# Optimization experiments

Hardware: AMD Instinct MI355X
Metric: run time of the kernel (lower is better)

The kernel has to match this reference:

```python
import jax, jax.numpy as jnp
import numpy as np

N = 50000   # nodes
E = 800000  # edges (avg degree 16)
IN = 128
HID = 128
OUT = 64    # num classes


def setup_inputs() -> dict:
    key = jax.random.key(0)
    ks = jax.random.split(key, 10)
    x = jax.random.normal(ks[0], (N, IN), dtype=jnp.float32)
    edge_src = jax.random.randint(ks[1], (E,), 0, N)
    edge_dst = jax.random.randint(ks[2], (E,), 0, N)
    y = jax.random.randint(ks[3], (N,), 0, OUT)
    train_mask = jax.random.bernoulli(ks[4], 0.5, (N,))
    w = lambda k, sh: (jax.random.normal(k, sh, dtype=jnp.float32) * (1.0 / np.sqrt(sh[0]))).astype(jnp.float32)
    return dict(
        x=x, edge_src=edge_src, edge_dst=edge_dst, y=y, train_mask=train_mask,
        W1l=w(ks[5], (IN, HID)), b1=jnp.zeros((HID,), jnp.float32), W1r=w(ks[6], (IN, HID)),
        W2l=w(ks[7], (HID, OUT)), b2=jnp.zeros((OUT,), jnp.float32), W2r=w(ks[8], (HID, OUT)),
    )


def mean_aggr(h, src, dst, n):
    # sparse adjacency matmul with reduce='mean': for each dst node, mean of src features
    msg_sum = jax.ops.segment_sum(h[src], dst, num_segments=n)          # [N, D]
    cnt = jax.ops.segment_sum(jnp.ones((src.shape[0],), h.dtype), dst, num_segments=n)
    return msg_sum / jnp.maximum(cnt, 1.0)[:, None]


def reference(x, edge_src, edge_dst, y, train_mask, W1l, b1, W1r, W2l, b2, W2r):
    n = x.shape[0]
    # dropout(p=0.2, training=False) is identity in eval mode
    h = x
    # layer 1: SAGEConv = lin_l(mean_aggr(h)) + lin_r(h), then ReLU (+identity dropout)
    a = mean_aggr(h, edge_src, edge_dst, n)
    h = jax.nn.relu(a @ W1l + b1 + h @ W1r)
    # layer 2 (output layer)
    a = mean_aggr(h, edge_src, edge_dst, n)
    logits = a @ W2l + b2 + h @ W2r
    logp = jax.nn.log_softmax(logits, axis=1)
    # nll_loss over masked nodes (single chunk => loss / num_chunks with num_chunks=1)
    m = train_mask.astype(logp.dtype)
    nll = -jnp.take_along_axis(logp, y[:, None], axis=1)[:, 0]
    loss = jnp.sum(nll * m) / jnp.maximum(jnp.sum(m), 1.0)
    return loss
```

## Files before the change

### kernel.cpp

```cpp
#include <hip/hip_runtime.h>
#include <hip/hip_bf16.h>

typedef unsigned int uint;
typedef unsigned short u16;

#define DIN 128
#define DHID 128
#define DOUT 64
#define BSH 8
#define P3CHUNK 8192
#define P4MAX 6144

static inline size_t al256(size_t x) { return (x + 255) & ~(size_t)255; }

typedef __attribute__((ext_vector_type(8))) short short8;
typedef __attribute__((ext_vector_type(4))) float floatx4;
typedef __attribute__((ext_vector_type(2))) float floatx2;
typedef __attribute__((ext_vector_type(4))) int intx4;

__device__ inline float2 bf2x(uint v) {
    return make_float2(__uint_as_float(v << 16), __uint_as_float(v & 0xffff0000u));
}
__device__ inline uint packbf(float a, float b) {
    uint ua = __float_as_uint(a), ub = __float_as_uint(b);
    ua += 0x7fff + ((ua >> 16) & 1);
    ub += 0x7fff + ((ub >> 16) & 1);
    return (ua >> 16) | (ub & 0xffff0000u);
}
__device__ inline u16 pb(float a) {
    uint u = __float_as_uint(a);
    u += 0x7fff + ((u >> 16) & 1);
    return (u16)(u >> 16);
}

__device__ inline floatx2 f8lo(uint v) {
#if __has_builtin(__builtin_amdgcn_cvt_pk_f32_fp8)
    return __builtin_amdgcn_cvt_pk_f32_fp8((int)v, false);
#else
    uint b0 = v & 0xffu, b1 = (v >> 8) & 0xffu;
    floatx2 r;
    r.x = __uint_as_float(((b0 & 0x80u) << 24) | ((b0 & 0x7fu) << 20)) * 0x1p120f;
    r.y = __uint_as_float(((b1 & 0x80u) << 24) | ((b1 & 0x7fu) << 20)) * 0x1p120f;
    return r;
#endif
}
__device__ inline floatx2 f8hi(uint v) {
#if __has_builtin(__builtin_amdgcn_cvt_pk_f32_fp8)
    return __builtin_amdgcn_cvt_pk_f32_fp8((int)v, true);
#else
    uint b0 = (v >> 16) & 0xffu, b1 = (v >> 24) & 0xffu;
    floatx2 r;
    r.x = __uint_as_float(((b0 & 0x80u) << 24) | ((b0 & 0x7fu) << 20)) * 0x1p120f;
    r.y = __uint_as_float(((b1 & 0x80u) << 24) | ((b1 & 0x7fu) << 20)) * 0x1p120f;
    return r;
#endif
}
__device__ inline uint enc8(float f) {
    uint ub = __float_as_uint(f * 0x1p-120f);
    uint s = (ub >> 24) & 0x80u;
    uint mag = ub & 0x7fffffffu;
    mag += 0x7ffffu + ((mag >> 20) & 1u);
    uint r = mag >> 20;
    if (r > 0x7eu) r = 0x7eu;
    return r | s;
}
__device__ inline uint packf8x4(float a, float b, float c, float d) {
#if __has_builtin(__builtin_amdgcn_cvt_pk_fp8_f32)
    int p = __builtin_amdgcn_cvt_pk_fp8_f32(a, b, 0, false);
    p = __builtin_amdgcn_cvt_pk_fp8_f32(c, d, p, true);
    return (uint)p;
#else
    return enc8(a) | (enc8(b) << 8) | (enc8(c) << 16) | (enc8(d) << 24);
#endif
}

__global__ __launch_bounds__(256) void pack_detect_bhist_kernel(
    const float* __restrict__ W1l, const float* __restrict__ W1r,
    const float* __restrict__ W2l, const float* __restrict__ W2r,
    u16* __restrict__ Wp1, u16* __restrict__ Wp2,
    const int* __restrict__ tm, int n_int, int* __restrict__ gflags,
    const int* __restrict__ dst, int e, int nb, uint* __restrict__ bcounts) {
    __shared__ uint lh[512];
    int bx = blockIdx.x;
    if (bx < 192) {
        int id = bx * 256 + threadIdx.x;
        if (id < 32768) {
            int frag = id >> 9, el = id & 511;
            int lane = el >> 3, j = el & 7;
            int kc = frag >> 4, tn = frag & 15;
            int k = kc * 32 + (lane >> 4) * 8 + j;
            int ncol = tn * 16 + (lane & 15);
            float v = (ncol < 128) ? W1l[k * 128 + ncol] : W1r[k * 128 + ncol - 128];
            Wp1[id] = pb(v);
        } else if (id < 49152) {
            int id2 = id - 32768;
            int frag = id2 >> 9, el = id2 & 511;
            int lane = el >> 3, j = el & 7;
            int kc = frag >> 3, tn = frag & 7;
            int k = kc * 32 + (lane >> 4) * 8 + j;
            int ncol = tn * 16 + (lane & 15);
            float v = (ncol < 64) ? W2l[k * 64 + ncol] : W2r[k * 64 + ncol - 64];
            Wp2[id2] = pb(v);
        }
    } else if (bx < 256) {
        int i = (bx - 192) * 256 + threadIdx.x;
        bool hf = false, ho = false;
        for (; i < n_int; i += 64 * 256) {
            int v = tm[i];
            hf |= (v == 0x3F800000);
            ho |= (v != 0 && v != 1 && v != 0x3F800000);
        }
        if (__any(hf) && (threadIdx.x & 63) == 0) atomicOr(&gflags[0], 1);
        if (__any(ho) && (threadIdx.x & 63) == 0) atomicOr(&gflags[1], 1);
    } else {
        for (int i = threadIdx.x; i < 512; i += 256) lh[i] = 0;
        __syncthreads();
        int nquad = (e + 3) >> 2;
        for (int i = (bx - 256) * 256 + threadIdx.x; i < nquad; i += 256 * 256) {
            int base = i * 4;
            if (base + 4 <= e) {
                intx4 d = __builtin_nontemporal_load((const intx4*)(dst + base));
                atomicAdd(&lh[d.x >> BSH], 1u);
                atomicAdd(&lh[d.y >> BSH], 1u);
                atomicAdd(&lh[d.z >> BSH], 1u);
                atomicAdd(&lh[d.w >> BSH], 1u);
            } else {
                for (int k = base; k < e; ++k) atomicAdd(&lh[dst[k] >> BSH], 1u);
            }
        }
        __syncthreads();
        for (int i = threadIdx.x; i < nb; i += 256) {
            uint c = lh[i];
            if (c) atomicAdd(&bcounts[i], c);
        }
    }
}

__global__ __launch_bounds__(256) void bscan_kernel(const uint* __restrict__ bcounts, int nb, int e,
                                                    uint* __restrict__ bbase, uint* __restrict__ bcursor,
                                                    int* __restrict__ offsets, int n) {
    __shared__ uint pws[4];
    int t = threadIdx.x;
    uint v0 = (2 * t < nb) ? bcounts[2 * t] : 0u;
    uint v1 = (2 * t + 1 < nb) ? bcounts[2 * t + 1] : 0u;
    uint s = v0 + v1;
    int lane = t & 63, wv = t >> 6;
    uint incl = s;
    #pragma unroll
    for (int d = 1; d < 64; d <<= 1) {
        uint u = (uint)__shfl_up((int)incl, d, 64);
        if (lane >= d) incl += u;
    }
    if (lane == 63) pws[wv] = incl;
    __syncthreads();
    uint woff = 0;
    #pragma unroll
    for (int i = 0; i < 4; ++i) if (i < wv) woff += pws[i];
    uint excl = woff + incl - s;
    if (2 * t < nb) { bbase[2 * t] = excl; bcursor[2 * t] = excl; }
    if (2 * t + 1 < nb) { bbase[2 * t + 1] = excl + v0; bcursor[2 * t + 1] = excl + v0; }
    if (t == 0) {
        uint tot = pws[0] + pws[1] + pws[2] + pws[3];
        bbase[nb] = tot;
        offsets[n] = e;
    }
}

__global__ __launch_bounds__(256) void partition_kernel(const int* __restrict__ src,
                                                        const int* __restrict__ dst, int e, int nb,
                                                        uint* __restrict__ bcursor,
                                                        uint* __restrict__ pairs) {
    __shared__ uint lh[512], lexcl[512], lbase[512], lpos[512];
    __shared__ uint st[P3CHUNK];
    __shared__ uint pws[4];
    int t = threadIdx.x;
    int e0 = blockIdx.x * P3CHUNK;
    int ecnt = min(P3CHUNK, e - e0);
    for (int i = t; i < 512; i += 256) { lh[i] = 0; lpos[i] = 0; }
    __syncthreads();
    for (int i = t; i < ecnt; i += 256)
        atomicAdd(&lh[dst[e0 + i] >> BSH], 1u);
    __syncthreads();
    {
        uint v0 = lh[2 * t], v1 = lh[2 * t + 1];
        uint s = v0 + v1;
        int lane = t & 63, wv = t >> 6;
        uint incl = s;
        #pragma unroll
        for (int d = 1; d < 64; d <<= 1) {
            uint u = (uint)__shfl_up((int)incl, d, 64);
            if (lane >= d) incl += u;
        }
        if (lane == 63) pws[wv] = incl;
        __syncthreads();
        uint woff = 0;
        #pragma unroll
        for (int i = 0; i < 4; ++i) if (i < wv) woff += pws[i];
        uint excl = woff + incl - s;
        lexcl[2 * t] = excl;
        lexcl[2 * t + 1] = excl + v0;
    }
    __syncthreads();
    for (int b = t; b < nb; b += 256) {
        uint c = lh[b];
        lbase[b] = c ? atomicAdd(&bcursor[b], c) : 0u;
    }
    __syncthreads();
    for (int i = t; i < ecnt; i += 256) {
        int d = dst[e0 + i];
        int s = src[e0 + i];
        int b = d >> BSH;
        uint slot = lexcl[b] + atomicAdd(&lpos[b], 1u);
        st[slot] = ((uint)(d & ((1 << BSH) - 1)) << 16) | (uint)s;
    }
    __syncthreads();
    int wv = t >> 6, lane = t & 63;
    for (int b = wv; b < nb; b += 4) {
        uint c = lh[b];
        uint lsrc = lexcl[b], gdst = lbase[b];
        for (uint k = lane; k < c; k += 64)
            pairs[gdst + k] = st[lsrc + k];
    }
}

__global__ __launch_bounds__(256) void emit_gemm1_kernel(
    const uint* __restrict__ pairs, const uint* __restrict__ bbase,
    u16* __restrict__ csr, int* __restrict__ offsets, int nb_emit,
    const float* __restrict__ X, const u16* __restrict__ Wp1,
    const float* __restrict__ b1,
    uint* __restrict__ P1f8, uint* __restrict__ Q1u, int n) {
    __shared__ u16 smem[4][16][260];
    int t = threadIdx.x;
    if (blockIdx.x < nb_emit) {
        uint* cnt = (uint*)&smem[0][0][0];
        uint* lex = cnt + 256;
        uint* pws = lex + 256;
        u16* ob = (u16*)(pws + 8);
        int b = blockIdx.x;
        uint seg0 = bbase[b];
        int len = (int)(bbase[b + 1] - seg0);
        int n0 = b << BSH;
        cnt[t] = 0;
        __syncthreads();
        for (int i = t; i < len; i += 256)
            atomicAdd(&cnt[pairs[seg0 + i] >> 16], 1u);
        __syncthreads();
        uint v = cnt[t];
        int lane = t & 63, wv = t >> 6;
        uint incl = v;
        #pragma unroll
        for (int d = 1; d < 64; d <<= 1) {
            uint u = (uint)__shfl_up((int)incl, d, 64);
            if (lane >= d) incl += u;
        }
        if (lane == 63) pws[wv] = incl;
        __syncthreads();
        uint woff = 0;
        #pragma unroll
        for (int i = 0; i < 4; ++i) if (i < wv) woff += pws[i];
        uint excl = woff + incl - v;
        lex[t] = excl;
        if (n0 + t < n) offsets[n0 + t] = (int)(seg0 + excl);
        __syncthreads();
        cnt[t] = 0;
        __syncthreads();
        for (int i = t; i < len; i += 256) {
            uint p = pairs[seg0 + i];
            uint loc = p >> 16;
            uint slot = lex[loc] + atomicAdd(&cnt[loc], 1u);
            if (slot < P4MAX) ob[slot] = (u16)(p & 0xffffu);
            else csr[seg0 + slot] = (u16)(p & 0xffffu);
        }
        __syncthreads();
        int lim = min(len, P4MAX);
        for (int i = t; i < lim; i += 256) csr[seg0 + i] = ob[i];
        return;
    }
    int bid = blockIdx.x - nb_emit;
    int w = t >> 6, lane = t & 63;
    int q = lane >> 4, c = lane & 15;
    int m0 = bid * 128 + w * 32;
    int meA = min(m0 + c, n - 1);
    int meB = min(m0 + 16 + c, n - 1);
    const float* xrowA = X + (size_t)meA * 128 + q * 8;
    const float* xrowB = X + (size_t)meB * 128 + q * 8;
    const u16* wbase = Wp1 + lane * 8;

    floatx4 acc[2][16];
    #pragma unroll
    for (int h = 0; h < 2; ++h)
        #pragma unroll
        for (int i = 0; i < 16; ++i) acc[h][i] = (floatx4){0.f, 0.f, 0.f, 0.f};

    #pragma unroll
    for (int kc = 0; kc < 4; ++kc) {
        float4 xa0 = *(const float4*)(xrowA + kc * 32);
        float4 xa1 = *(const float4*)(xrowA + kc * 32 + 4);
        float4 xb0 = *(const float4*)(xrowB + kc * 32);
        float4 xb1 = *(const float4*)(xrowB + kc * 32 + 4);
        union { short8 s; uint4 u; } a0, a1;
        a0.u.x = packbf(xa0.x, xa0.y); a0.u.y = packbf(xa0.z, xa0.w);
        a0.u.z = packbf(xa1.x, xa1.y); a0.u.w = packbf(xa1.z, xa1.w);
        a1.u.x = packbf(xb0.x, xb0.y); a1.u.y = packbf(xb0.z, xb0.w);
        a1.u.z = packbf(xb1.x, xb1.y); a1.u.w = packbf(xb1.z, xb1.w);
        #pragma unroll
        for (int tn = 0; tn < 16; ++tn) {
            union { short8 s; uint4 u; } b;
            b.u = *(const uint4*)(wbase + (kc * 16 + tn) * 512);
            acc[0][tn] = __builtin_amdgcn_mfma_f32_16x16x32_bf16(a0.s, b.s, acc[0][tn], 0, 0, 0);
            acc[1][tn] = __builtin_amdgcn_mfma_f32_16x16x32_bf16(a1.s, b.s, acc[1][tn], 0, 0, 0);
        }
    }

    #pragma unroll
    for (int h = 0; h < 2; ++h) {
        #pragma unroll
        for (int tn = 0; tn < 16; ++tn) {
            int col = tn * 16 + c;
            float badd = (tn >= 8) ? b1[col - 128] : 0.f;
            #pragma unroll
            for (int i = 0; i < 4; ++i)
                smem[w][q * 4 + i][col] = pb(acc[h][tn][i] + badd);
        }
        int r0 = m0 + h * 16;
        for (int r = 0; r < 16; ++r) {
            int grow = r0 + r;
            if (grow >= n) continue;
            uint2 v = *(const uint2*)&smem[w][r][lane * 4];
            if (lane < 32) {
                float2 e0 = bf2x(v.x), e1 = bf2x(v.y);
                P1f8[(size_t)grow * 32 + lane] = packf8x4(e0.x, e0.y, e1.x, e1.y);
            } else {
                *(uint2*)&Q1u[(size_t)grow * 64 + 2 * (lane - 32)] = v;
            }
        }
    }
}

__global__ __launch_bounds__(256) void hist_kernel(const int* __restrict__ dst, int e,
                                                   int* __restrict__ counts) {
    int base = (blockIdx.x * 256 + threadIdx.x) * 4;
    if (base + 4 <= e) {
        intx4 d = __builtin_nontemporal_load((const intx4*)(dst + base));
        atomicAdd(&counts[d.x], 1);
        atomicAdd(&counts[d.y], 1);
        atomicAdd(&counts[d.z], 1);
        atomicAdd(&counts[d.w], 1);
    } else {
        for (int i = base; i < e; ++i) atomicAdd(&counts[dst[i]], 1);
    }
}

__global__ __launch_bounds__(256) void scan_partial_kernel(const int* __restrict__ counts, int n,
                                                           int* __restrict__ partials) {
    int t = threadIdx.x;
    int base = blockIdx.x * 1024 + t * 4;
    int s = 0;
    if (base + 3 < n) {
        int4 v = *(const int4*)&counts[base];
        s = v.x + v.y + v.z + v.w;
    } else {
        for (int i = 0; i < 4; ++i) if (base + i < n) s += counts[base + i];
    }
    #pragma unroll
    for (int d = 32; d; d >>= 1) s += __shfl_down(s, d, 64);
    __shared__ int wsum[4];
    if ((t & 63) == 0) wsum[t >> 6] = s;
    __syncthreads();
    if (t == 0) partials[blockIdx.x] = wsum[0] + wsum[1] + wsum[2] + wsum[3];
}

__global__ void scan_top_kernel(int* __restrict__ partials, int nparts, int* __restrict__ total_out) {
    int lane = threadIdx.x;
    int v = (lane < nparts) ? partials[lane] : 0;
    int incl = v;
    #pragma unroll
    for (int d = 1; d < 64; d <<= 1) {
        int u = __shfl_up(incl, d, 64);
        if (lane >= d) incl += u;
    }
    if (lane < nparts) partials[lane] = incl - v;
    if (lane == 63) *total_out = incl;
}

__global__ __launch_bounds__(256) void scan_final_kernel(const int* __restrict__ counts, int n,
                                                         const int* __restrict__ partials,
                                                         int* __restrict__ offsets,
                                                         int* __restrict__ cursor) {
    int t = threadIdx.x;
    int base = blockIdx.x * 1024 + t * 4;
    int v0 = 0, v1 = 0, v2 = 0, v3 = 0;
    if (base + 3 < n) {
        int4 q = *(const int4*)&counts[base];
        v0 = q.x; v1 = q.y; v2 = q.z; v3 = q.w;
    } else {
        if (base + 0 < n) v0 = counts[base + 0];
        if (base + 1 < n) v1 = counts[base + 1];
        if (base + 2 < n) v2 = counts[base + 2];
        if (base + 3 < n) v3 = counts[base + 3];
    }
    int s = v0 + v1 + v2 + v3;
    int lane = t & 63, wid = t >> 6;
    int incl = s;
    #pragma unroll
    for (int d = 1; d < 64; d <<= 1) {
        int u = __shfl_up(incl, d, 64);
        if (lane >= d) incl += u;
    }
    __shared__ int wsum[4];
    if (lane == 63) wsum[wid] = incl;
    __syncthreads();
    int woff = 0;
    #pragma unroll
    for (int i = 0; i < 4; ++i) if (i < wid) woff += wsum[i];
    int run = partials[blockIdx.x] + woff + incl - s;
    if (base + 0 < n) { offsets[base + 0] = run; cursor[base + 0] = run; run += v0; }
    if (base + 1 < n) { offsets[base + 1] = run; cursor[base + 1] = run; run += v1; }
    if (base + 2 < n) { offsets[base + 2] = run; cursor[base + 2] = run; run += v2; }
    if (base + 3 < n) { offsets[base + 3] = run; cursor[base + 3] = run; run += v3; }
}

__global__ __launch_bounds__(256) void scatter_kernel(const int* __restrict__ src,
                                                      const int* __restrict__ dst, int e,
                                                      int* __restrict__ cursor,
                                                      uint* __restrict__ csr_src) {
    int base = (blockIdx.x * 256 + threadIdx.x) * 4;
    if (base + 4 <= e) {
        intx4 s = __builtin_nontemporal_load((const intx4*)(src + base));
        intx4 d = __builtin_nontemporal_load((const intx4*)(dst + base));
        int p0 = atomicAdd(&cursor[d.x], 1);
        int p1 = atomicAdd(&cursor[d.y], 1);
        int p2 = atomicAdd(&cursor[d.z], 1);
        int p3 = atomicAdd(&cursor[d.w], 1);
        csr_src[p0] = (uint)s.x;
        csr_src[p1] = (uint)s.y;
        csr_src[p2] = (uint)s.z;
        csr_src[p3] = (uint)s.w;
    } else {
        for (int i = base; i < e; ++i) {
            int p = atomicAdd(&cursor[dst[i]], 1);
            csr_src[p] = (uint)src[i];
        }
    }
}

template <typename IT>
__global__ __launch_bounds__(256) void aggr1_kernel(
    const uint* __restrict__ P1f8, const uint* __restrict__ Q1u,
    const int* __restrict__ offsets, const IT* __restrict__ csr,
    uint* __restrict__ h1u, int n) {
    int node = (int)((blockIdx.x * (size_t)blockDim.x + threadIdx.x) >> 6);
    int lane = threadIdx.x & 63;
    int l = lane & 31, hw = lane >> 5;
    if (node >= n) return;
    int beg = offsets[node], end = offsets[node + 1];
    float a0 = 0.f, a1 = 0.f, a2 = 0.f, a3 = 0.f;
    int i = beg + hw;
    for (; i + 6 < end; i += 8) {
        int s0 = csr[i], s1 = csr[i + 2], s2 = csr[i + 4], s3 = csr[i + 6];
        uint v0 = P1f8[(size_t)s0 * 32 + l];
        uint v1 = P1f8[(size_t)s1 * 32 + l];
        uint v2 = P1f8[(size_t)s2 * 32 + l];
        uint v3 = P1f8[(size_t)s3 * 32 + l];
        floatx2 u0 = f8lo(v0), w0 = f8hi(v0);
        floatx2 u1 = f8lo(v1), w1 = f8hi(v1);
        floatx2 u2 = f8lo(v2), w2 = f8hi(v2);
        floatx2 u3 = f8lo(v3), w3 = f8hi(v3);
        a0 += (u0.x + u1.x) + (u2.x + u3.x);
        a1 += (u0.y + u1.y) + (u2.y + u3.y);
        a2 += (w0.x + w1.x) + (w2.x + w3.x);
        a3 += (w0.y + w1.y) + (w2.y + w3.y);
    }
    for (; i < end; i += 2) {
        int s = csr[i];
        uint v = P1f8[(size_t)s * 32 + l];
        floatx2 u = f8lo(v), w2 = f8hi(v);
        a0 += u.x; a1 += u.y; a2 += w2.x; a3 += w2.y;
    }
    a0 += __shfl_xor(a0, 32, 64);
    a1 += __shfl_xor(a1, 32, 64);
    a2 += __shfl_xor(a2, 32, 64);
    a3 += __shfl_xor(a3, 32, 64);
    if (hw == 0) {
        float inv = 1.0f / (float)max(end - beg, 1);
        uint2 qv = *(const uint2*)&Q1u[(size_t)node * 64 + l * 2];
        float2 q0 = bf2x(qv.x), q1 = bf2x(qv.y);
        float r0 = fmaxf(fmaf(a0, inv, q0.x), 0.f);
        float r1 = fmaxf(fmaf(a1, inv, q0.y), 0.f);
        float r2 = fmaxf(fmaf(a2, inv, q1.x), 0.f);
        float r3 = fmaxf(fmaf(a3, inv, q1.y), 0.f);
        uint2 o;
        o.x = packbf(r0, r1);
        o.y = packbf(r2, r3);
        *(uint2*)&h1u[(size_t)node * 64 + l * 2] = o;
    }
}

__global__ __launch_bounds__(256) void gemm2_mfma(
    const uint* __restrict__ H1u, const u16* __restrict__ Wp2,
    const float* __restrict__ b2,
    uint* __restrict__ P2f8, uint* __restrict__ Q2u, int n) {
    __shared__ u16 ep[4][16][132];
    int t = threadIdx.x;
    int w = t >> 6, lane = t & 63;
    int q = lane >> 4, c = lane & 15;
    int m0 = blockIdx.x * 128 + w * 32;
    int meA = min(m0 + c, n - 1);
    int meB = min(m0 + 16 + c, n - 1);
    const u16* hrowA = (const u16*)H1u + (size_t)meA * 128 + q * 8;
    const u16* hrowB = (const u16*)H1u + (size_t)meB * 128 + q * 8;
    const u16* wbase = Wp2 + lane * 8;

    floatx4 acc[2][8];
    #pragma unroll
    for (int h = 0; h < 2; ++h)
        #pragma unroll
        for (int i = 0; i < 8; ++i) acc[h][i] = (floatx4){0.f, 0.f, 0.f, 0.f};

    #pragma unroll
    for (int kc = 0; kc < 4; ++kc) {
        union { short8 s; uint4 u; } a0, a1;
        a0.u = *(const uint4*)(hrowA + kc * 32);
        a1.u = *(const uint4*)(hrowB + kc * 32);
        #pragma unroll
        for (int tn = 0; tn < 8; ++tn) {
            union { short8 s; uint4 u; } b;
            b.u = *(const uint4*)(wbase + (kc * 8 + tn) * 512);
            acc[0][tn] = __builtin_amdgcn_mfma_f32_16x16x32_bf16(a0.s, b.s, acc[0][tn], 0, 0, 0);
            acc[1][tn] = __builtin_amdgcn_mfma_f32_16x16x32_bf16(a1.s, b.s, acc[1][tn], 0, 0, 0);
        }
    }

    #pragma unroll
    for (int h = 0; h < 2; ++h) {
        #pragma unroll
        for (int tn = 0; tn < 8; ++tn) {
            int col = tn * 16 + c;
            float badd = (tn >= 4) ? b2[col - 64] : 0.f;
            #pragma unroll
            for (int i = 0; i < 4; ++i)
                ep[w][q * 4 + i][col] = pb(acc[h][tn][i] + badd);
        }
        int r0 = m0 + h * 16;
        for (int r = 0; r < 16; ++r) {
            int grow = r0 + r;
            if (grow >= n) continue;
            if (lane < 16) {
                uint2 v = *(const uint2*)&ep[w][r][lane * 4];
                float2 e0 = bf2x(v.x), e1 = bf2x(v.y);
                P2f8[(size_t)grow * 16 + lane] = packf8x4(e0.x, e0.y, e1.x, e1.y);
            } else if (lane < 48) {
                uint v = *(const uint*)&ep[w][r][64 + (lane - 16) * 2];
                Q2u[(size_t)grow * 32 + (lane - 16)] = v;
            }
        }
    }
}

template <typename IT>
__global__ __launch_bounds__(1024) void loss_kernel(
    const uint* __restrict__ P2f8, const uint* __restrict__ Q2u,
    const int* __restrict__ offsets, const IT* __restrict__ csr,
    const int* __restrict__ y, const void* __restrict__ tmask,
    const int* __restrict__ gflags, float2* __restrict__ bpart, int n) {
    __shared__ int sflag;
    if (threadIdx.x == 0) sflag = gflags[0] ? 2 : (gflags[1] ? 0 : 1);
    int wid = threadIdx.x >> 6;
    int node = blockIdx.x * 16 + wid;
    int lane = threadIdx.x & 63;
    int l = lane & 15, qw = lane >> 4;
    __syncthreads();
    float num = 0.f, den = 0.f;
    if (node < n) {
        int beg = offsets[node], end = offsets[node + 1];
        float a0 = 0.f, a1 = 0.f, a2 = 0.f, a3 = 0.f;
        int i = beg + qw;
        for (; i + 4 < end; i += 8) {
            int s0 = csr[i], s1 = csr[i + 4];
            uint v0 = P2f8[(size_t)s0 * 16 + l];
            uint v1 = P2f8[(size_t)s1 * 16 + l];
            floatx2 u0 = f8lo(v0), w0 = f8hi(v0);
            floatx2 u1 = f8lo(v1), w1 = f8hi(v1);
            a0 += u0.x + u1.x; a1 += u0.y + u1.y;
            a2 += w0.x + w1.x; a3 += w0.y + w1.y;
        }
        for (; i < end; i += 4) {
            int s = csr[i];
            uint v = P2f8[(size_t)s * 16 + l];
            floatx2 u = f8lo(v), w2 = f8hi(v);
            a0 += u.x; a1 += u.y; a2 += w2.x; a3 += w2.y;
        }
        #pragma unroll
        for (int d = 16; d <= 32; d <<= 1) {
            a0 += __shfl_xor(a0, d, 64);
            a1 += __shfl_xor(a1, d, 64);
            a2 += __shfl_xor(a2, d, 64);
            a3 += __shfl_xor(a3, d, 64);
        }
        float inv = 1.0f / (float)max(end - beg, 1);
        uint2 qv = *(const uint2*)&Q2u[(size_t)node * 32 + l * 2];
        float2 q0 = bf2x(qv.x), q1 = bf2x(qv.y);
        float L0 = fmaf(a0, inv, q0.x);
        float L1 = fmaf(a1, inv, q0.y);
        float L2 = fmaf(a2, inv, q1.x);
        float L3 = fmaf(a3, inv, q1.y);
        float mx = fmaxf(fmaxf(L0, L1), fmaxf(L2, L3));
        #pragma unroll
        for (int d = 1; d <= 8; d <<= 1) mx = fmaxf(mx, __shfl_xor(mx, d, 64));
        float s = __expf(L0 - mx) + __expf(L1 - mx) + __expf(L2 - mx) + __expf(L3 - mx);
        #pragma unroll
        for (int d = 1; d <= 8; d <<= 1) s += __shfl_xor(s, d, 64);
        int cls = y[node];
        int srcl = (cls >> 2) & 15;
        float c0 = __shfl(L0, srcl, 64);
        float c1 = __shfl(L1, srcl, 64);
        float c2 = __shfl(L2, srcl, 64);
        float c3 = __shfl(L3, srcl, 64);
        int sel = cls & 3;
        float Lc = (sel == 0) ? c0 : (sel == 1) ? c1 : (sel == 2) ? c2 : c3;
        float logp = (Lc - mx) - __logf(s);
        int f = sflag;
        bool m;
        if (f == 0)      m = ((const unsigned char*)tmask)[node] != 0;
        else if (f == 1) m = ((const int*)tmask)[node] != 0;
        else             m = ((const float*)tmask)[node] != 0.f;
        if (m) { num = -logp; den = 1.f; }
    }
    __shared__ float2 wacc[16];
    if (lane == 0) wacc[wid] = make_float2(num, den);
    __syncthreads();
    if (threadIdx.x == 0) {
        float rx = 0.f, ry = 0.f;
        #pragma unroll
        for (int i = 0; i < 16; ++i) { rx += wacc[i].x; ry += wacc[i].y; }
        bpart[blockIdx.x] = make_float2(rx, ry);
    }
}

__global__ __launch_bounds__(1024) void finalize_kernel(const float2* __restrict__ bpart, int nb,
                                                        float* __restrict__ out) {
    int t = threadIdx.x;
    float sx = 0.f, sy = 0.f;
    for (int i = t; i < nb; i += 1024) { float2 v = bpart[i]; sx += v.x; sy += v.y; }
    #pragma unroll
    for (int d = 32; d; d >>= 1) { sx += __shfl_down(sx, d, 64); sy += __shfl_down(sy, d, 64); }
    __shared__ float2 wacc[16];
    if ((t & 63) == 0) wacc[t >> 6] = make_float2(sx, sy);
    __syncthreads();
    if (t == 0) {
        float nx = 0.f, ny = 0.f;
        #pragma unroll
        for (int i = 0; i < 16; ++i) { nx += wacc[i].x; ny += wacc[i].y; }
        out[0] = nx / fmaxf(ny, 1.f);
    }
}

extern "C" void kernel_launch(void* const* d_in, const int* in_sizes, int n_in,
                              void* d_out, int out_size, void* d_ws, size_t ws_size,
                              hipStream_t stream) {
    const float* x        = (const float*)d_in[0];
    const int*   edge_src = (const int*)d_in[1];
    const int*   edge_dst = (const int*)d_in[2];
    const int*   y        = (const int*)d_in[3];
    const void*  tmask    = (const void*)d_in[4];
    const float* W1l      = (const float*)d_in[5];
    const float* b1       = (const float*)d_in[6];
    const float* W1r      = (const float*)d_in[7];
    const float* W2l      = (const float*)d_in[8];
    const float* b2       = (const float*)d_in[9];
    const float* W2r      = (const float*)d_in[10];

    const int N = in_sizes[0] / DIN;
    const int E = in_sizes[1];
    const int nb_loss = (N + 15) / 16;
    const bool small_idx = (N <= 65535);
    const int nb = (N + 255) >> BSH;

    char* ws = (char*)d_ws;
    int* gflags = (int*)ws;
    size_t off = 256;
    uint* bcounts = (uint*)(ws + off); off += al256(513 * 4);
    uint* bbase   = (uint*)(ws + off); off += al256(513 * 4);
    uint* bcursor = (uint*)(ws + off); off += al256(513 * 4);
    int* offsets  = (int*)(ws + off); off += al256(((size_t)N + 1) * 4);
    uint* pairs   = (uint*)(ws + off); off += al256((size_t)E * 4);
    void* csr     = (void*)(ws + off); off += al256((size_t)E * 4);
    int* counts   = (int*)(ws + off); off += al256((size_t)N * 4);
    int* cursor   = (int*)(ws + off); off += al256((size_t)N * 4);
    int* spart    = (int*)(ws + off); off += al256(64 * 4);
    float2* bpart = (float2*)(ws + off); off += al256((size_t)nb_loss * 8);
    u16* Wp1      = (u16*)(ws + off); off += al256(32768 * 2);
    u16* Wp2      = (u16*)(ws + off); off += al256(16384 * 2);
    uint* P1f8    = (uint*)(ws + off); off += al256((size_t)N * 32 * 4);
    uint* h1u     = (uint*)(ws + off); off += al256((size_t)N * 64 * 4);
    uint* Q1u     = (uint*)(ws + off); off += al256((size_t)N * 64 * 4);
    uint* P2f8    = Q1u;
    uint* Q2u     = Q1u + (size_t)N * 16;

    hipMemsetAsync(ws, 0, 8192, stream);

    int gb32 = (N + 127) / 128;

    if (small_idx) {
        pack_detect_bhist_kernel<<<512, 256, 0, stream>>>(
            W1l, W1r, W2l, W2r, Wp1, Wp2, (const int*)tmask, N / 4, gflags,
            edge_dst, E, nb, bcounts);
        bscan_kernel<<<1, 256, 0, stream>>>(bcounts, nb, E, bbase, bcursor, offsets, N);
        int pblocks = (E + P3CHUNK - 1) / P3CHUNK;
        partition_kernel<<<pblocks, 256, 0, stream>>>(edge_src, edge_dst, E, nb, bcursor, pairs);
        emit_gemm1_kernel<<<nb + gb32, 256, 0, stream>>>(
            pairs, bbase, (u16*)csr, offsets, nb, x, Wp1, b1, P1f8, Q1u, N);
        int ab = (N + 3) / 4;
        aggr1_kernel<u16><<<ab, 256, 0, stream>>>(P1f8, Q1u, offsets, (const u16*)csr, h1u, N);
        gemm2_mfma<<<gb32, 256, 0, stream>>>(h1u, Wp2, b2, P2f8, Q2u, N);
        loss_kernel<u16><<<nb_loss, 1024, 0, stream>>>(
            P2f8, Q2u, offsets, (const u16*)csr, y, tmask, gflags, bpart, N);
    } else {
        pack_detect_bhist_kernel<<<256, 256, 0, stream>>>(
            W1l, W1r, W2l, W2r, Wp1, Wp2, (const int*)tmask, N / 4, gflags,
            edge_dst, E, nb, bcounts);
        hipMemsetAsync(counts, 0, (size_t)N * 4, stream);
        int eb4 = (E + 1023) / 1024;
        hist_kernel<<<eb4, 256, 0, stream>>>(edge_dst, E, counts);
        int sb = (N + 1023) / 1024;
        scan_partial_kernel<<<sb, 256, 0, stream>>>(counts, N, spart);
        scan_top_kernel<<<1, 64, 0, stream>>>(spart, sb, &offsets[N]);
        scan_final_kernel<<<sb, 256, 0, stream>>>(counts, N, spart, offsets, cursor);
        scatter_kernel<<<eb4, 256, 0, stream>>>(edge_src, edge_dst, E, cursor, (uint*)csr);
        emit_gemm1_kernel<<<gb32, 256, 0, stream>>>(
            pairs, bbase, (u16*)csr, offsets, 0, x, Wp1, b1, P1f8, Q1u, N);
        int ab = (N + 3) / 4;
        aggr1_kernel<uint><<<ab, 256, 0, stream>>>(P1f8, Q1u, offsets, (const uint*)csr, h1u, N);
        gemm2_mfma<<<gb32, 256, 0, stream>>>(h1u, Wp2, b2, P2f8, Q2u, N);
        loss_kernel<uint><<<nb_loss, 1024, 0, stream>>>(
            P2f8, Q2u, offsets, (const uint*)csr, y, tmask, gflags, bpart, N);
    }
    finalize_kernel<<<1, 1024, 0, stream>>>(bpart, nb_loss, (float*)d_out);
}
```

Measured before the change: 232.9 us.

## Fuse bucket scan into partition, co-schedule GEMM1 with partition, split emit

Removes the single-block bucket scan kernel. Each partition block now recomputes the global bucket prefix from bcounts and adds it to an atomic cursor that starts at zero, since the workspace memset already clears it. The layer-1 GEMM blocks now run in the same launch as the partition blocks instead of alongside CSR emit, and emit becomes its own kernel that also recomputes bucket bases. The goal is one fewer launch and better overlap of the compute-heavy GEMM with the atomic-heavy partition. In exchange, the scans are repeated in every block, and the GEMM blocks now reserve the larger shared buffer, which may lower their occupancy.

```diff
diff --git a/kernel.cpp b/kernel.cpp
--- a/kernel.cpp
+++ b/kernel.cpp
@@ -136,147 +136,94 @@
     }
 }
 
-__global__ __launch_bounds__(256) void bscan_kernel(const uint* __restrict__ bcounts, int nb, int e,
-                                                    uint* __restrict__ bbase, uint* __restrict__ bcursor,
-                                                    int* __restrict__ offsets, int n) {
-    __shared__ uint pws[4];
-    int t = threadIdx.x;
-    uint v0 = (2 * t < nb) ? bcounts[2 * t] : 0u;
-    uint v1 = (2 * t + 1 < nb) ? bcounts[2 * t + 1] : 0u;
-    uint s = v0 + v1;
-    int lane = t & 63, wv = t >> 6;
-    uint incl = s;
-    #pragma unroll
-    for (int d = 1; d < 64; d <<= 1) {
-        uint u = (uint)__shfl_up((int)incl, d, 64);
-        if (lane >= d) incl += u;
-    }
-    if (lane == 63) pws[wv] = incl;
-    __syncthreads();
-    uint woff = 0;
-    #pragma unroll
-    for (int i = 0; i < 4; ++i) if (i < wv) woff += pws[i];
-    uint excl = woff + incl - s;
-    if (2 * t < nb) { bbase[2 * t] = excl; bcursor[2 * t] = excl; }
-    if (2 * t + 1 < nb) { bbase[2 * t + 1] = excl + v0; bcursor[2 * t + 1] = excl + v0; }
-    if (t == 0) {
-        uint tot = pws[0] + pws[1] + pws[2] + pws[3];
-        bbase[nb] = tot;
-        offsets[n] = e;
-    }
-}
-
-__global__ __launch_bounds__(256) void partition_kernel(const int* __restrict__ src,
-                                                        const int* __restrict__ dst, int e, int nb,
-                                                        uint* __restrict__ bcursor,
-                                                        uint* __restrict__ pairs) {
-    __shared__ uint lh[512], lexcl[512], lbase[512], lpos[512];
-    __shared__ uint st[P3CHUNK];
-    __shared__ uint pws[4];
-    int t = threadIdx.x;
-    int e0 = blockIdx.x * P3CHUNK;
-    int ecnt = min(P3CHUNK, e - e0);
-    for (int i = t; i < 512; i += 256) { lh[i] = 0; lpos[i] = 0; }
-    __syncthreads();
-    for (int i = t; i < ecnt; i += 256)
-        atomicAdd(&lh[dst[e0 + i] >> BSH], 1u);
-    __syncthreads();
-    {
-        uint v0 = lh[2 * t], v1 = lh[2 * t + 1];
-        uint s = v0 + v1;
-        int lane = t & 63, wv = t >> 6;
-        uint incl = s;
-        #pragma unroll
-        for (int d = 1; d < 64; d <<= 1) {
-            uint u = (uint)__shfl_up((int)incl, d, 64);
-            if (lane >= d) incl += u;
-        }
-        if (lane == 63) pws[wv] = incl;
-        __syncthreads();
-        uint woff = 0;
-        #pragma unroll
-        for (int i = 0; i < 4; ++i) if (i < wv) woff += pws[i];
-        uint excl = woff + incl - s;
-        lexcl[2 * t] = excl;
-        lexcl[2 * t + 1] = excl + v0;
-    }
-    __syncthreads();
-    for (int b = t; b < nb; b += 256) {
-        uint c = lh[b];
-        lbase[b] = c ? atomicAdd(&bcursor[b], c) : 0u;
-    }
-    __syncthreads();
-    for (int i = t; i < ecnt; i += 256) {
-        int d = dst[e0 + i];
-        int s = src[e0 + i];
-        int b = d >> BSH;
-        uint slot = lexcl[b] + atomicAdd(&lpos[b], 1u);
-        st[slot] = ((uint)(d & ((1 << BSH) - 1)) << 16) | (uint)s;
-    }
-    __syncthreads();
-    int wv = t >> 6, lane = t & 63;
-    for (int b = wv; b < nb; b += 4) {
-        uint c = lh[b];
-        uint lsrc = lexcl[b], gdst = lbase[b];
-        for (uint k = lane; k < c; k += 64)
-            pairs[gdst + k] = st[lsrc + k];
-    }
-}
-
-__global__ __launch_bounds__(256) void emit_gemm1_kernel(
-    const uint* __restrict__ pairs, const uint* __restrict__ bbase,
-    u16* __restrict__ csr, int* __restrict__ offsets, int nb_emit,
+__global__ __launch_bounds__(256) void partition_gemm1_kernel(
+    const int* __restrict__ src, const int* __restrict__ dst, int e, int nb,
+    const uint* __restrict__ bcounts, uint* __restrict__ bcursor,
+    uint* __restrict__ pairs, int npart,
     const float* __restrict__ X, const u16* __restrict__ Wp1,
     const float* __restrict__ b1,
     uint* __restrict__ P1f8, uint* __restrict__ Q1u, int n) {
-    __shared__ u16 smem[4][16][260];
+    __shared__ uint sbuf[10248];
     int t = threadIdx.x;
-    if (blockIdx.x < nb_emit) {
-        uint* cnt = (uint*)&smem[0][0][0];
-        uint* lex = cnt + 256;
-        uint* pws = lex + 256;
-        u16* ob = (u16*)(pws + 8);
-        int b = blockIdx.x;
-        uint seg0 = bbase[b];
-        int len = (int)(bbase[b + 1] - seg0);
-        int n0 = b << BSH;
-        cnt[t] = 0;
-        __syncthreads();
-        for (int i = t; i < len; i += 256)
-            atomicAdd(&cnt[pairs[seg0 + i] >> 16], 1u);
-        __syncthreads();
-        uint v = cnt[t];
-        int lane = t & 63, wv = t >> 6;
-        uint incl = v;
-        #pragma unroll
-        for (int d = 1; d < 64; d <<= 1) {
-            uint u = (uint)__shfl_up((int)incl, d, 64);
-            if (lane >= d) incl += u;
-        }
-        if (lane == 63) pws[wv] = incl;
-        __syncthreads();
-        uint woff = 0;
-        #pragma unroll
-        for (int i = 0; i < 4; ++i) if (i < wv) woff += pws[i];
-        uint excl = woff + incl - v;
-        lex[t] = excl;
-        if (n0 + t < n) offsets[n0 + t] = (int)(seg0 + excl);
-        __syncthreads();
-        cnt[t] = 0;
-        __syncthreads();
-        for (int i = t; i < len; i += 256) {
-            uint p = pairs[seg0 + i];
-            uint loc = p >> 16;
-            uint slot = lex[loc] + atomicAdd(&cnt[loc], 1u);
-            if (slot < P4MAX) ob[slot] = (u16)(p & 0xffffu);
-            else csr[seg0 + slot] = (u16)(p & 0xffffu);
-        }
-        __syncthreads();
-        int lim = min(len, P4MAX);
-        for (int i = t; i < lim; i += 256) csr[seg0 + i] = ob[i];
+    if (blockIdx.x < npart) {
+        uint* lh    = sbuf;
+        uint* lexcl = sbuf + 512;
+        uint* lbase = sbuf + 1024;
+        uint* lpos  = sbuf + 1536;
+        uint* pws   = sbuf + 2048;
+        uint* st    = sbuf + 2056;
+        int e0 = blockIdx.x * P3CHUNK;
+        int ecnt = min(P3CHUNK, e - e0);
+        for (int i = t; i < 512; i += 256) { lh[i] = 0; lpos[i] = 0; }
+        __syncthreads();
+        for (int i = t; i < ecnt; i += 256)
+            atomicAdd(&lh[dst[e0 + i] >> BSH], 1u);
+        __syncthreads();
+        {
+            uint v0 = lh[2 * t], v1 = lh[2 * t + 1];
+            uint s = v0 + v1;
+            int lane = t & 63, wv = t >> 6;
+            uint incl = s;
+            #pragma unroll
+            for (int d = 1; d < 64; d <<= 1) {
+                uint u = (uint)__shfl_up((int)incl, d, 64);
+                if (lane >= d) incl += u;
+            }
+            if (lane == 63) pws[wv] = incl;
+            __syncthreads();
+            uint woff = 0;
+            #pragma unroll
+            for (int i = 0; i < 4; ++i) if (i < wv) woff += pws[i];
+            uint excl = woff + incl - s;
+            lexcl[2 * t] = excl;
+            lexcl[2 * t + 1] = excl + v0;
+        }
+        __syncthreads();
+        {
+            uint v0 = (2 * t < nb) ? bcounts[2 * t] : 0u;
+            uint v1 = (2 * t + 1 < nb) ? bcounts[2 * t + 1] : 0u;
+            uint s = v0 + v1;
+            int lane = t & 63, wv = t >> 6;
+            uint incl = s;
+            #pragma unroll
+            for (int d = 1; d < 64; d <<= 1) {
+                uint u = (uint)__shfl_up((int)incl, d, 64);
+                if (lane >= d) incl += u;
+            }
+            if (lane == 63) pws[wv] = incl;
+            __syncthreads();
+            uint woff = 0;
+            #pragma unroll
+            for (int i = 0; i < 4; ++i) if (i < wv) woff += pws[i];
+            uint excl = woff + incl - s;
+            if (2 * t < nb) lbase[2 * t] = excl;
+            if (2 * t + 1 < nb) lbase[2 * t + 1] = excl + v0;
+        }
+        __syncthreads();
+        for (int b = t; b < nb; b += 256) {
+            uint c = lh[b];
+            if (c) lbase[b] += atomicAdd(&bcursor[b], c);
+        }
+        __syncthreads();
+        for (int i = t; i < ecnt; i += 256) {
+            int d = dst[e0 + i];
+            int s = src[e0 + i];
+            int b = d >> BSH;
+            uint slot = lexcl[b] + atomicAdd(&lpos[b], 1u);
+            st[slot] = ((uint)(d & ((1 << BSH) - 1)) << 16) | (uint)s;
+        }
+        __syncthreads();
+        int wv = t >> 6, lane = t & 63;
+        for (int b = wv; b < nb; b += 4) {
+            uint c = lh[b];
+            uint lsrc = lexcl[b], gdst = lbase[b];
+            for (uint k = lane; k < c; k += 64)
+                pairs[gdst + k] = st[lsrc + k];
+        }
         return;
     }
-    int bid = blockIdx.x - nb_emit;
+    u16* ep = (u16*)sbuf;
+    int bid = blockIdx.x - npart;
     int w = t >> 6, lane = t & 63;
     int q = lane >> 4, c = lane & 15;
     int m0 = bid * 128 + w * 32;
@@ -320,13 +267,13 @@
             float badd = (tn >= 8) ? b1[col - 128] : 0.f;
             #pragma unroll
             for (int i = 0; i < 4; ++i)
-                smem[w][q * 4 + i][col] = pb(acc[h][tn][i] + badd);
+                ep[((size_t)w * 16 + (q * 4 + i)) * 260 + col] = pb(acc[h][tn][i] + badd);
         }
         int r0 = m0 + h * 16;
         for (int r = 0; r < 16; ++r) {
             int grow = r0 + r;
             if (grow >= n) continue;
-            uint2 v = *(const uint2*)&smem[w][r][lane * 4];
+            uint2 v = *(const uint2*)&ep[((size_t)w * 16 + r) * 260 + lane * 4];
             if (lane < 32) {
                 float2 e0 = bf2x(v.x), e1 = bf2x(v.y);
                 P1f8[(size_t)grow * 32 + lane] = packf8x4(e0.x, e0.y, e1.x, e1.y);
@@ -335,6 +282,74 @@
             }
         }
     }
+}
+
+__global__ __launch_bounds__(256) void emit_kernel(const uint* __restrict__ pairs,
+                                                   const uint* __restrict__ bcounts, int nb,
+                                                   int e, int n,
+                                                   u16* __restrict__ csr, int* __restrict__ offsets) {
+    __shared__ uint cnt[256], lex[256], gb[512], pws[8];
+    __shared__ u16 ob[P4MAX];
+    int b = blockIdx.x, t = threadIdx.x;
+    {
+        uint v0 = (2 * t < nb) ? bcounts[2 * t] : 0u;
+        uint v1 = (2 * t + 1 < nb) ? bcounts[2 * t + 1] : 0u;
+        uint s = v0 + v1;
+        int lane = t & 63, wv = t >> 6;
+        uint incl = s;
+        #pragma unroll
+        for (int d = 1; d < 64; d <<= 1) {
+            uint u = (uint)__shfl_up((int)incl, d, 64);
+            if (lane >= d) incl += u;
+        }
+        if (lane == 63) pws[wv] = incl;
+        __syncthreads();
+        uint woff = 0;
+        #pragma unroll
+        for (int i = 0; i < 4; ++i) if (i < wv) woff += pws[i];
+        uint excl = woff + incl - s;
+        if (2 * t < nb) gb[2 * t] = excl;
+        if (2 * t + 1 < nb) gb[2 * t + 1] = excl + v0;
+    }
+    __syncthreads();
+    uint seg0 = gb[b];
+    int len = (int)bcounts[b];
+    int n0 = b << BSH;
+    if (b == 0 && t == 0) offsets[n] = e;
+    cnt[t] = 0;
+    __syncthreads();
+    for (int i = t; i < len; i += 256)
+        atomicAdd(&cnt[pairs[seg0 + i] >> 16], 1u);
+    __syncthreads();
+    uint v = cnt[t];
+    int lane = t & 63, wv = t >> 6;
+    uint incl = v;
+    #pragma unroll
+    for (int d = 1; d < 64; d <<= 1) {
+        uint u = (uint)__shfl_up((int)incl, d, 64);
+        if (lane >= d) incl += u;
+    }
+    if (lane == 63) pws[wv] = incl;
+    __syncthreads();
+    uint woff = 0;
+    #pragma unroll
+    for (int i = 0; i < 4; ++i) if (i < wv) woff += pws[i];
+    uint excl = woff + incl - v;
+    lex[t] = excl;
+    if (n0 + t < n) offsets[n0 + t] = (int)(seg0 + excl);
+    __syncthreads();
+    cnt[t] = 0;
+    __syncthreads();
+    for (int i = t; i < len; i += 256) {
+        uint p = pairs[seg0 + i];
+        uint loc = p >> 16;
+        uint slot = lex[loc] + atomicAdd(&cnt[loc], 1u);
+        if (slot < P4MAX) ob[slot] = (u16)(p & 0xffffu);
+        else csr[seg0 + slot] = (u16)(p & 0xffffu);
+    }
+    __syncthreads();
+    int lim = min(len, P4MAX);
+    for (int i = t; i < lim; i += 256) csr[seg0 + i] = ob[i];
 }
 
 __global__ __launch_bounds__(256) void hist_kernel(const int* __restrict__ dst, int e,
@@ -680,7 +695,6 @@
     int* gflags = (int*)ws;
     size_t off = 256;
     uint* bcounts = (uint*)(ws + off); off += al256(513 * 4);
-    uint* bbase   = (uint*)(ws + off); off += al256(513 * 4);
     uint* bcursor = (uint*)(ws + off); off += al256(513 * 4);
     int* offsets  = (int*)(ws + off); off += al256(((size_t)N + 1) * 4);
     uint* pairs   = (uint*)(ws + off); off += al256((size_t)E * 4);
@@ -705,11 +719,11 @@
         pack_detect_bhist_kernel<<<512, 256, 0, stream>>>(
             W1l, W1r, W2l, W2r, Wp1, Wp2, (const int*)tmask, N / 4, gflags,
             edge_dst, E, nb, bcounts);
-        bscan_kernel<<<1, 256, 0, stream>>>(bcounts, nb, E, bbase, bcursor, offsets, N);
         int pblocks = (E + P3CHUNK - 1) / P3CHUNK;
-        partition_kernel<<<pblocks, 256, 0, stream>>>(edge_src, edge_dst, E, nb, bcursor, pairs);
-        emit_gemm1_kernel<<<nb + gb32, 256, 0, stream>>>(
-            pairs, bbase, (u16*)csr, offsets, nb, x, Wp1, b1, P1f8, Q1u, N);
+        partition_gemm1_kernel<<<pblocks + gb32, 256, 0, stream>>>(
+            edge_src, edge_dst, E, nb, bcounts, bcursor, pairs, pblocks,
+            x, Wp1, b1, P1f8, Q1u, N);
+        emit_kernel<<<nb, 256, 0, stream>>>(pairs, bcounts, nb, E, N, (u16*)csr, offsets);
         int ab = (N + 3) / 4;
         aggr1_kernel<u16><<<ab, 256, 0, stream>>>(P1f8, Q1u, offsets, (const u16*)csr, h1u, N);
         gemm2_mfma<<<gb32, 256, 0, stream>>>(h1u, Wp2, b2, P2f8, Q2u, N);
@@ -727,8 +741,9 @@
         scan_top_kernel<<<1, 64, 0, stream>>>(spart, sb, &offsets[N]);
         scan_final_kernel<<<sb, 256, 0, stream>>>(counts, N, spart, offsets, cursor);
         scatter_kernel<<<eb4, 256, 0, stream>>>(edge_src, edge_dst, E, cursor, (uint*)csr);
-        emit_gemm1_kernel<<<gb32, 256, 0, stream>>>(
-            pairs, bbase, (u16*)csr, offsets, 0, x, Wp1, b1, P1f8, Q1u, N);
+        partition_gemm1_kernel<<<gb32, 256, 0, stream>>>(
+            edge_src, edge_dst, E, nb, bcounts, bcursor, pairs, 0,
+            x, Wp1, b1, P1f8, Q1u, N);
         int ab = (N + 3) / 4;
         aggr1_kernel<uint><<<ab, 256, 0, stream>>>(P1f8, Q1u, offsets, (const uint*)csr, h1u, N);
         gemm2_mfma<<<gb32, 256, 0, stream>>>(h1u, Wp2, b2, P2f8, Q2u, N);
```

Result: faster. 213.8 us (-8.2%).
